# Kernel tuning notes

Measured on AMD Instinct MI355X. Metric: run time of the kernel, lower is better.

## Reference

```python
import jax, jax.numpy as jnp
import numpy as np

B, S, E, H, D, W = 2, 4096, 768, 12, 64, 256  # batch, seq, hidden, heads, head_dim, one-sided window


def setup_inputs() -> dict:
    key = jax.random.key(0)
    ks = jax.random.split(key, 4)
    s = 0.02
    return {
        "hidden_states": jax.random.normal(ks[0], (B, S, E), jnp.float32),
        "Wq": jax.random.normal(ks[1], (E, E), jnp.float32) * s,
        "bq": jnp.zeros((E,), jnp.float32),
        "Wk": jax.random.normal(ks[2], (E, E), jnp.float32) * s,
        "bk": jnp.zeros((E,), jnp.float32),
        "Wv": jax.random.normal(ks[3], (E, E), jnp.float32) * s,
        "bv": jnp.zeros((E,), jnp.float32),
    }


def _band_attention(q, k, v):
    # q,k,v: [B,H,S,D]. Sliding-window attention: query i attends keys j with |j-i| <= W,
    # clipped to [0, S) -- same math as sliding_chunks_matmul_qk + mask_invalid_locations
    # + softmax + sliding_chunks_matmul_pv (dropout p=0, eval mode).
    C = S // W  # number of query chunks of size W

    def ext(x):
        # gather, for each chunk c, the keys of chunks c-1, c, c+1 (zero padded at edges)
        xp = jnp.pad(x, ((0, 0), (0, 0), (W, W), (0, 0)))
        xc = xp.reshape(B, H, C + 2, W, D)
        return jnp.concatenate([xc[:, :, 0:C], xc[:, :, 1:C + 1], xc[:, :, 2:C + 2]], axis=3)  # [B,H,C,3W,D]

    qc = q.reshape(B, H, C, W, D)
    ke = ext(k)
    ve = ext(v)
    scores = jnp.einsum('bhcpd,bhctd->bhcpt', qc, ke)  # [B,H,C,W,3W]

    p = jnp.arange(W)[:, None]            # query offset within chunk
    t = jnp.arange(3 * W)[None, :]        # key offset within extended window
    rel = t - W - p                       # j - i  (relative position)
    j = jnp.arange(C)[:, None, None] * W + (t - W)[None]  # global key index [C,W,3W]
    mask = (jnp.abs(rel)[None] <= W) & (j >= 0) & (j < S)  # band + sequence-boundary mask

    scores = jnp.where(mask[None, None], scores, -1e30)
    probs = jax.nn.softmax(scores, axis=-1)
    out = jnp.einsum('bhcpt,bhctd->bhcpd', probs, ve)
    return out.reshape(B, H, S, D)


def reference(hidden_states, Wq, bq, Wk, bk, Wv, bv):
    scale = 1.0 / float(np.sqrt(D))
    q = (hidden_states @ Wq + bq) * scale  # q scaled by 1/sqrt(head_dim) as in original
    k = hidden_states @ Wk + bk
    v = hidden_states @ Wv + bv
    split = lambda x: x.reshape(B, S, H, D).transpose(0, 2, 1, 3)  # [B,H,S,D]
    out = _band_attention(split(q), split(k), split(v))
    return out.transpose(0, 2, 1, 3).reshape(B, S, E)  # [B,S,E] context_layer
```

## Files before the change

### kernel.cpp

```cpp
#include <hip/hip_runtime.h>

#define BB 2
#define SS 4096
#define EE 768
#define HH 12
#define DD 64
#define WW 256

typedef __attribute__((ext_vector_type(8))) short short8;
typedef __attribute__((ext_vector_type(4))) short short4v;
typedef __attribute__((ext_vector_type(4))) float floatx4;

#define MFMA16(a, b, c) __builtin_amdgcn_mfma_f32_16x16x32_bf16(a, b, c, 0, 0, 0)

__device__ __forceinline__ float bf2f(short x) {
    union { unsigned u; float f; } v;
    v.u = ((unsigned)(unsigned short)x) << 16;
    return v.f;
}

__device__ __forceinline__ short f2bf(float x) {
    union { float f; unsigned u; } v;
    v.f = x;
    unsigned r = v.u + 0x7fffu + ((v.u >> 16) & 1u);
    return (short)(r >> 16);
}

__device__ __forceinline__ float exp2_fast(float x) {
    float r;
    asm("v_exp_f32 %0, %1" : "=v"(r) : "v"(x));
    return r;
}

__device__ __forceinline__ int imin(int a, int b) { return a < b ? a : b; }
__device__ __forceinline__ int imax(int a, int b) { return a > b ? a : b; }

__device__ __forceinline__ void gload_lds16(const short* g, short* l) {
    __builtin_amdgcn_global_load_lds(
        (const __attribute__((address_space(1))) unsigned*)g,
        (__attribute__((address_space(3))) unsigned*)l, 16, 0, 0);
}

__global__ __launch_bounds__(256) void prep(
    const float* __restrict__ hidden, const float* __restrict__ W0,
    const float* __restrict__ W1, const float* __restrict__ W2,
    short* __restrict__ Xb, short* __restrict__ Wt) {
    __shared__ short t[32][33];
    int bid = blockIdx.x;
    int tid = threadIdx.x;
    if (bid < 6144) {
        size_t i4 = (size_t)bid * 256 + tid;
        floatx4 f = *(const floatx4*)(hidden + i4 * 4);
        short4v s;
#pragma unroll
        for (int k = 0; k < 4; k++) s[k] = f2bf(f[k]);
        *(short4v*)(Xb + i4 * 4) = s;
    } else {
        int tmp = bid - 6144;
        int z = tmp / 576, r = tmp % 576;
        int bx = r % 24, by = r / 24;
        const float* in = (z == 0) ? W0 : (z == 1) ? W1 : W2;
        short* op = Wt + (size_t)z * EE * EE;
        int y0 = by * 32;
        int ty = tid >> 3, tx4 = tid & 7;
        floatx4 f = *(const floatx4*)&in[(size_t)(y0 + ty) * EE + bx * 32 + tx4 * 4];
#pragma unroll
        for (int k = 0; k < 4; k++) t[ty][tx4 * 4 + k] = f2bf(f[k]);
        __syncthreads();
        int A = tid >> 3, B0 = (tid & 7) * 4;
        short4v v;
#pragma unroll
        for (int k = 0; k < 4; k++) v[k] = t[B0 + k][A];
        *(short4v*)&op[(size_t)(bx * 32 + A) * EE + y0 + B0] = v;
    }
}

__global__ __launch_bounds__(512) void qkv_gemm(
    const short* __restrict__ Xb, const short* __restrict__ Wt,
    const float* __restrict__ Bq, const float* __restrict__ Bk, const float* __restrict__ Bv,
    short* __restrict__ Qo, short* __restrict__ Ko, short* __restrict__ Vto) {
    int z = blockIdx.z;
    const short* Wz = Wt + (size_t)z * EE * EE;
    const float* bias = (z == 0) ? Bq : (z == 1) ? Bk : Bv;

    __shared__ __align__(16) short As[3][256 * 32];
    __shared__ __align__(16) short Bs[3][128 * 32];
    int tid = threadIdx.x;
    int m0 = blockIdx.x * 256, n0 = blockIdx.y * 128;
    int wave = tid >> 6, lane = tid & 63, lquad = lane >> 4, lrow = lane & 15;
    int wm = (wave >> 1) * 64, wn = (wave & 1) * 64;

    floatx4 acc[4][4] = {};

    int c0 = tid, c1 = 512 + tid;
    int u0 = (c0 & 7) ^ ((c0 >> 3) & 7);
    int r0s = (c0 >> 3) * 2 + (u0 >> 2), q0s = (u0 & 3) * 8;

    const short* xa0 = &Xb[(size_t)(m0 + r0s) * EE + q0s];
    const short* xa1 = xa0 + (size_t)128 * EE;
    const short* wb0 = &Wz[(size_t)(n0 + r0s) * EE + q0s];

    auto issueTile = [&](int t) {
        int k0 = t * 32;
        int bs = t % 3;
        gload_lds16(xa0 + k0, &As[bs][c0 * 8]);
        gload_lds16(xa1 + k0, &As[bs][c1 * 8]);
        gload_lds16(wb0 + k0, &Bs[bs][c0 * 8]);
    };

    int offA[4], offB[4];
#pragma unroll
    for (int mt = 0; mt < 4; mt++) {
        int ra = wm + mt * 16 + lrow;
        int sa = (lquad | ((ra & 1) << 2)) ^ ((ra >> 1) & 7);
        offA[mt] = (ra >> 1) * 64 + sa * 8;
        int rb = wn + mt * 16 + lrow;
        int sb = (lquad | ((rb & 1) << 2)) ^ ((rb >> 1) & 7);
        offB[mt] = (rb >> 1) * 64 + sb * 8;
    }

    issueTile(0);
    issueTile(1);

#pragma unroll
    for (int t = 0; t < 24; ++t) {
        if (t < 23) asm volatile("s_waitcnt vmcnt(3)" ::: "memory");
        else        asm volatile("s_waitcnt vmcnt(0)" ::: "memory");
        __builtin_amdgcn_sched_barrier(0);
        __builtin_amdgcn_s_barrier();
        asm volatile("" ::: "memory");

        if (t + 2 < 24) issueTile(t + 2);

        int bs = t % 3;
        short8 af[4], bfv[4];
#pragma unroll
        for (int mt = 0; mt < 4; mt++)
            af[mt] = *(short8*)&As[bs][offA[mt]];
#pragma unroll
        for (int nt = 0; nt < 4; nt++)
            bfv[nt] = *(short8*)&Bs[bs][offB[nt]];
#pragma unroll
        for (int mt = 0; mt < 4; mt++)
#pragma unroll
            for (int nt = 0; nt < 4; nt++)
                acc[mt][nt] = MFMA16(af[mt], bfv[nt], acc[mt][nt]);
    }

    if (z == 2) {
        for (int nt = 0; nt < 4; nt++) {
            int gn = n0 + wn + nt * 16 + lrow;
            float bv = bias[gn];
            int h = gn >> 6, d = gn & 63;
            for (int mt = 0; mt < 4; mt++) {
                int gm0 = m0 + wm + mt * 16 + lquad * 4;
                int b = gm0 >> 12, s = gm0 & (SS - 1);
                short4v pk;
                for (int r = 0; r < 4; r++) pk[r] = f2bf(acc[mt][nt][r] + bv);
                *(short4v*)&Vto[(((size_t)(b * HH + h)) * DD + d) * SS + s] = pk;
            }
        }
    } else {
        short* out = (z == 0) ? Qo : Ko;
        float scale = (z == 0) ? 0.125f * 1.44269504088896f : 1.0f;
        for (int nt = 0; nt < 4; nt++) {
            int gn = n0 + wn + nt * 16 + lrow;
            float bv = bias[gn];
            int h = gn >> 6, d = gn & 63;
            for (int mt = 0; mt < 4; mt++) {
                int gmb = m0 + wm + mt * 16 + lquad * 4;
                for (int r = 0; r < 4; r++) {
                    int gm = gmb + r;
                    int b = gm >> 12, s = gm & (SS - 1);
                    float v = (acc[mt][nt][r] + bv) * scale;
                    out[(((size_t)(b * HH + h)) * SS + s) * DD + d] = f2bf(v);
                }
            }
        }
    }
}

__global__ __launch_bounds__(256) void band_attn(
    const short* __restrict__ Q, const short* __restrict__ K,
    const short* __restrict__ Vt, float* __restrict__ out) {
    int hb = blockIdx.x;
    int h = hb % HH, b = hb / HH;
    int chunk = blockIdx.y;
    int tid = threadIdx.x;
    int wave = tid >> 6, lane = tid & 63, lquad = lane >> 4, lrow = lane & 15;
    int qbase = chunk * 128 + wave * 32;

    const short* Qh = Q + ((size_t)(b * HH + h)) * SS * DD;
    const short* Kh = K + ((size_t)(b * HH + h)) * SS * DD;
    const short* Vh = Vt + ((size_t)(b * HH + h)) * DD * SS;

    __shared__ __align__(16) short Ks[2][64 * 72];
    __shared__ __align__(16) short Vs[2][64 * 72];
    __shared__ __align__(16) short Ps[4][16 * 72];
    short* Pw = &Ps[wave][0];

    short8 qf[2][2];
#pragma unroll
    for (int m = 0; m < 2; m++)
#pragma unroll
        for (int hh = 0; hh < 2; hh++)
            qf[m][hh] = *(const short8*)&Qh[(size_t)(qbase + m * 16 + lrow) * DD + hh * 32 + lquad * 8];

    floatx4 o[2][4] = {};
    float ls[2] = {0.0f, 0.0f};

    int kwin = chunk * 128 - WW;
    int srow = tid >> 3;
    int scol = (tid & 7) * 8;
    int tlo = wave >> 1;

    short8 kreg[2], vreg[2];
    auto loadTile = [&](int t) {
        int ks0 = kwin + t * 64;
#pragma unroll
        for (int i = 0; i < 2; i++) {
            int r = srow + i * 32;
            int gk = imin(imax(ks0 + r, 0), SS - 1);
            kreg[i] = *(const short8*)&Kh[(size_t)gk * DD + scol];
            int gv = imin(imax(ks0 + scol, 0), SS - 8);
            vreg[i] = *(const short8*)&Vh[(size_t)r * SS + gv];
        }
    };
    auto storeTile = [&](int buf) {
#pragma unroll
        for (int i = 0; i < 2; i++) {
            int r = srow + i * 32;
            *(short8*)&Ks[buf][r * 72 + scol] = kreg[i];
            *(short8*)&Vs[buf][r * 72 + scol] = vreg[i];
        }
    };

    loadTile(0);
    storeTile(0);
    __syncthreads();

    for (int t = 0; t < 10; t++) {
        int buf = t & 1;
        if (t < 9) loadTile(t + 1);

        if ((unsigned)(t - tlo) < 9u) {
            int ks0 = kwin + t * 64;
            short8 kf[4][2], vf[4][2];
#pragma unroll
            for (int kt = 0; kt < 4; kt++)
#pragma unroll
                for (int hh = 0; hh < 2; hh++)
                    kf[kt][hh] = *(short8*)&Ks[buf][(kt * 16 + lrow) * 72 + hh * 32 + lquad * 8];
#pragma unroll
            for (int nt = 0; nt < 4; nt++)
#pragma unroll
                for (int hh = 0; hh < 2; hh++)
                    vf[nt][hh] = *(short8*)&Vs[buf][(nt * 16 + lrow) * 72 + hh * 32 + lquad * 8];

            int d0 = ks0 - qbase;
            bool interior = (d0 >= -225) && (d0 <= 193) && (ks0 >= 0) && (ks0 <= SS - 64);

            __builtin_amdgcn_s_setprio(1);
#pragma unroll
            for (int m = 0; m < 2; m++) {
                int q = qbase + m * 16 + lrow;
                floatx4 s[4];
#pragma unroll
                for (int kt = 0; kt < 4; kt++) {
                    floatx4 zz = {};
                    s[kt] = MFMA16(kf[kt][0], qf[m][0], zz);
                    s[kt] = MFMA16(kf[kt][1], qf[m][1], s[kt]);
                }
                float lacc = 0.0f;
                if (interior) {
#pragma unroll
                    for (int kt = 0; kt < 4; kt++) {
                        short4v pk;
#pragma unroll
                        for (int r = 0; r < 4; r++) {
                            float p = exp2_fast(s[kt][r]);
                            pk[r] = f2bf(p);
                            lacc += bf2f(pk[r]);
                        }
                        *(short4v*)&Pw[lrow * 72 + kt * 16 + lquad * 4] = pk;
                    }
                } else {
#pragma unroll
                    for (int kt = 0; kt < 4; kt++) {
                        short4v pk;
#pragma unroll
                        for (int r = 0; r < 4; r++) {
                            int key = ks0 + kt * 16 + lquad * 4 + r;
                            bool valid = ((unsigned)(key - q + WW) <= 2u * WW) && ((unsigned)key < SS);
                            float p = valid ? exp2_fast(s[kt][r]) : 0.0f;
                            pk[r] = f2bf(p);
                            lacc += bf2f(pk[r]);
                        }
                        *(short4v*)&Pw[lrow * 72 + kt * 16 + lquad * 4] = pk;
                    }
                }
                ls[m] += lacc;
                asm volatile("" ::: "memory");
                short8 ap0 = *(short8*)&Pw[lrow * 72 + lquad * 8];
                short8 ap1 = *(short8*)&Pw[lrow * 72 + 32 + lquad * 8];
#pragma unroll
                for (int nt = 0; nt < 4; nt++) {
                    o[m][nt] = MFMA16(ap0, vf[nt][0], o[m][nt]);
                    o[m][nt] = MFMA16(ap1, vf[nt][1], o[m][nt]);
                }
            }
            __builtin_amdgcn_s_setprio(0);
        }

        if (t < 9) storeTile(buf ^ 1);
        __syncthreads();
    }

#pragma unroll
    for (int m = 0; m < 2; m++) {
        ls[m] += __shfl_xor(ls[m], 16, 64);
        ls[m] += __shfl_xor(ls[m], 32, 64);
        ls[m] = 1.0f / ls[m];
    }

#pragma unroll
    for (int m = 0; m < 2; m++) {
#pragma unroll
        for (int r = 0; r < 4; r++) {
            float linv = __shfl(ls[m], lquad * 4 + r, 64);
            int s = qbase + m * 16 + lquad * 4 + r;
#pragma unroll
            for (int nt = 0; nt < 4; nt++)
                out[((size_t)b * SS + s) * EE + h * DD + nt * 16 + lrow] = o[m][nt][r] * linv;
        }
    }
}

extern "C" void kernel_launch(void* const* d_in, const int* in_sizes, int n_in,
                              void* d_out, int out_size, void* d_ws, size_t ws_size,
                              hipStream_t stream) {
    const float* hidden = (const float*)d_in[0];
    const float* Wq = (const float*)d_in[1];
    const float* bq = (const float*)d_in[2];
    const float* Wk = (const float*)d_in[3];
    const float* bk = (const float*)d_in[4];
    const float* Wv = (const float*)d_in[5];
    const float* bv = (const float*)d_in[6];
    float* out = (float*)d_out;

    short* ws = (short*)d_ws;
    const size_t WSZ = (size_t)EE * EE;
    const size_t QSZ = (size_t)BB * HH * SS * DD;
    short* Wt = ws;
    short* Qb = Wt + 3 * WSZ;
    short* Kb = Qb + QSZ;
    short* Vtb = Kb + QSZ;
    short* Xb = (short*)d_out;

    prep<<<dim3(6144 + 3 * 576, 1, 1), 256, 0, stream>>>(hidden, Wq, Wk, Wv, Xb, Wt);

    qkv_gemm<<<dim3(32, 6, 3), 512, 0, stream>>>(Xb, Wt, bq, bk, bv, Qb, Kb, Vtb);

    band_attn<<<dim3(HH * BB, SS / 128, 1), 256, 0, stream>>>(Qb, Kb, Vtb, out);
}
```

Measured before the change: 173.3 us.

## Use 64-wide K tiles with double buffering in QKV GEMM

The QKV projection GEMM now loads K-tiles of 64 instead of 32 and keeps two LDS buffers instead of three. The swizzle layout is simplified to row-major with an XOR on the 16-byte chunk index. The loop drops to 12 iterations, each waiting for all outstanding loads before computing. This halves the barrier count per tile and doubles the MFMA work between syncs, at the cost of a shallower prefetch depth (one tile ahead, full vmcnt(0) wait) and more LDS per block.

```diff
diff --git a/kernel.cpp b/kernel.cpp
--- a/kernel.cpp
+++ b/kernel.cpp
@@ -83,8 +83,8 @@
     const short* Wz = Wt + (size_t)z * EE * EE;
     const float* bias = (z == 0) ? Bq : (z == 1) ? Bk : Bv;
 
-    __shared__ __align__(16) short As[3][256 * 32];
-    __shared__ __align__(16) short Bs[3][128 * 32];
+    __shared__ __align__(16) short As[2][256 * 64];
+    __shared__ __align__(16) short Bs[2][128 * 64];
     int tid = threadIdx.x;
     int m0 = blockIdx.x * 256, n0 = blockIdx.y * 128;
     int wave = tid >> 6, lane = tid & 63, lquad = lane >> 4, lrow = lane & 15;
@@ -92,59 +92,64 @@
 
     floatx4 acc[4][4] = {};
 
-    int c0 = tid, c1 = 512 + tid;
-    int u0 = (c0 & 7) ^ ((c0 >> 3) & 7);
-    int r0s = (c0 >> 3) * 2 + (u0 >> 2), q0s = (u0 & 3) * 8;
-
-    const short* xa0 = &Xb[(size_t)(m0 + r0s) * EE + q0s];
-    const short* xa1 = xa0 + (size_t)128 * EE;
-    const short* wb0 = &Wz[(size_t)(n0 + r0s) * EE + q0s];
+    int r0 = tid >> 3, q0 = (tid & 7) ^ (r0 & 7);
+    const short* xa0 = &Xb[(size_t)(m0 + r0) * EE + q0 * 8];
+    const short* wb0 = &Wz[(size_t)(n0 + r0) * EE + q0 * 8];
+    int c0 = tid;
 
     auto issueTile = [&](int t) {
-        int k0 = t * 32;
-        int bs = t % 3;
-        gload_lds16(xa0 + k0, &As[bs][c0 * 8]);
-        gload_lds16(xa1 + k0, &As[bs][c1 * 8]);
-        gload_lds16(wb0 + k0, &Bs[bs][c0 * 8]);
+        int k0 = t * 64;
+        int bs = t & 1;
+        gload_lds16(xa0 + k0,            &As[bs][c0 * 8]);
+        gload_lds16(xa0 + 64 * EE + k0,  &As[bs][(c0 + 512) * 8]);
+        gload_lds16(xa0 + 128 * EE + k0, &As[bs][(c0 + 1024) * 8]);
+        gload_lds16(xa0 + 192 * EE + k0, &As[bs][(c0 + 1536) * 8]);
+        gload_lds16(wb0 + k0,            &Bs[bs][c0 * 8]);
+        gload_lds16(wb0 + 64 * EE + k0,  &Bs[bs][(c0 + 512) * 8]);
     };
 
-    int offA[4], offB[4];
+    int offA[4][2], offB[4][2];
 #pragma unroll
     for (int mt = 0; mt < 4; mt++) {
         int ra = wm + mt * 16 + lrow;
-        int sa = (lquad | ((ra & 1) << 2)) ^ ((ra >> 1) & 7);
-        offA[mt] = (ra >> 1) * 64 + sa * 8;
         int rb = wn + mt * 16 + lrow;
-        int sb = (lquad | ((rb & 1) << 2)) ^ ((rb >> 1) & 7);
-        offB[mt] = (rb >> 1) * 64 + sb * 8;
+#pragma unroll
+        for (int hh = 0; hh < 2; hh++) {
+            offA[mt][hh] = ra * 64 + ((hh * 4 + lquad) ^ (ra & 7)) * 8;
+            offB[mt][hh] = rb * 64 + ((hh * 4 + lquad) ^ (rb & 7)) * 8;
+        }
     }
 
     issueTile(0);
-    issueTile(1);
-
-#pragma unroll
-    for (int t = 0; t < 24; ++t) {
-        if (t < 23) asm volatile("s_waitcnt vmcnt(3)" ::: "memory");
-        else        asm volatile("s_waitcnt vmcnt(0)" ::: "memory");
+
+#pragma unroll
+    for (int t = 0; t < 12; ++t) {
+        asm volatile("s_waitcnt vmcnt(0)" ::: "memory");
         __builtin_amdgcn_sched_barrier(0);
         __builtin_amdgcn_s_barrier();
         asm volatile("" ::: "memory");
 
-        if (t + 2 < 24) issueTile(t + 2);
-
-        int bs = t % 3;
-        short8 af[4], bfv[4];
+        if (t + 1 < 12) issueTile(t + 1);
+
+        int bs = t & 1;
+        short8 af[4][2], bfv[4][2];
 #pragma unroll
         for (int mt = 0; mt < 4; mt++)
-            af[mt] = *(short8*)&As[bs][offA[mt]];
+#pragma unroll
+            for (int hh = 0; hh < 2; hh++)
+                af[mt][hh] = *(short8*)&As[bs][offA[mt][hh]];
 #pragma unroll
         for (int nt = 0; nt < 4; nt++)
-            bfv[nt] = *(short8*)&Bs[bs][offB[nt]];
+#pragma unroll
+            for (int hh = 0; hh < 2; hh++)
+                bfv[nt][hh] = *(short8*)&Bs[bs][offB[nt][hh]];
 #pragma unroll
         for (int mt = 0; mt < 4; mt++)
 #pragma unroll
-            for (int nt = 0; nt < 4; nt++)
-                acc[mt][nt] = MFMA16(af[mt], bfv[nt], acc[mt][nt]);
+            for (int nt = 0; nt < 4; nt++) {
+                acc[mt][nt] = MFMA16(af[mt][0], bfv[nt][0], acc[mt][nt]);
+                acc[mt][nt] = MFMA16(af[mt][1], bfv[nt][1], acc[mt][nt]);
+            }
     }
 
     if (z == 2) {
```

After: 181.2 us. 4.6% more time.

## Load K/V tiles directly into LDS with XOR-swizzled layout

Applied to the files above, without the earlier changes.

Replaces the register-staged global loads and LDS stores for K and V tiles with direct global-to-LDS loads (gload_lds16). The padded 72-stride layout is replaced by an XOR-swizzled 64-stride layout to avoid bank conflicts. The pipeline now waits on vmcnt and a barrier at the top of each iteration before issuing the next tile. This removes the VGPR staging and explicit LDS store instructions, but the prefetch now completes via a full vmcnt(0) wait each iteration.

```diff
diff --git a/kernel.cpp b/kernel.cpp
--- a/kernel.cpp
+++ b/kernel.cpp
@@ -194,8 +194,8 @@
     const short* Kh = K + ((size_t)(b * HH + h)) * SS * DD;
     const short* Vh = Vt + ((size_t)(b * HH + h)) * DD * SS;
 
-    __shared__ __align__(16) short Ks[2][64 * 72];
-    __shared__ __align__(16) short Vs[2][64 * 72];
+    __shared__ __align__(16) short Ks[2][64 * 64];
+    __shared__ __align__(16) short Vs[2][64 * 64];
     __shared__ __align__(16) short Ps[4][16 * 72];
     short* Pw = &Ps[wave][0];
 
@@ -210,52 +210,51 @@
     float ls[2] = {0.0f, 0.0f};
 
     int kwin = chunk * 128 - WW;
-    int srow = tid >> 3;
-    int scol = (tid & 7) * 8;
     int tlo = wave >> 1;
 
-    short8 kreg[2], vreg[2];
-    auto loadTile = [&](int t) {
+    int cr0 = tid >> 3, cq0 = (tid & 7) ^ (cr0 & 7);
+    int cr1 = (tid + 256) >> 3, cq1 = (tid & 7) ^ (cr1 & 7);
+
+    auto issueTile = [&](int t) {
         int ks0 = kwin + t * 64;
-#pragma unroll
-        for (int i = 0; i < 2; i++) {
-            int r = srow + i * 32;
-            int gk = imin(imax(ks0 + r, 0), SS - 1);
-            kreg[i] = *(const short8*)&Kh[(size_t)gk * DD + scol];
-            int gv = imin(imax(ks0 + scol, 0), SS - 8);
-            vreg[i] = *(const short8*)&Vh[(size_t)r * SS + gv];
-        }
+        int bs = t & 1;
+        int gk0 = imin(imax(ks0 + cr0, 0), SS - 1);
+        gload_lds16(&Kh[(size_t)gk0 * DD + cq0 * 8], &Ks[bs][tid * 8]);
+        int gk1 = imin(imax(ks0 + cr1, 0), SS - 1);
+        gload_lds16(&Kh[(size_t)gk1 * DD + cq1 * 8], &Ks[bs][(tid + 256) * 8]);
+        int gv0 = imin(imax(ks0 + cq0 * 8, 0), SS - 8);
+        gload_lds16(&Vh[(size_t)cr0 * SS + gv0], &Vs[bs][tid * 8]);
+        int gv1 = imin(imax(ks0 + cq1 * 8, 0), SS - 8);
+        gload_lds16(&Vh[(size_t)cr1 * SS + gv1], &Vs[bs][(tid + 256) * 8]);
     };
-    auto storeTile = [&](int buf) {
-#pragma unroll
-        for (int i = 0; i < 2; i++) {
-            int r = srow + i * 32;
-            *(short8*)&Ks[buf][r * 72 + scol] = kreg[i];
-            *(short8*)&Vs[buf][r * 72 + scol] = vreg[i];
-        }
-    };
-
-    loadTile(0);
-    storeTile(0);
-    __syncthreads();
+
+    int qx0 = lquad ^ (lrow & 7);
+    int qx1 = (4 + lquad) ^ (lrow & 7);
+
+    issueTile(0);
 
     for (int t = 0; t < 10; t++) {
-        int buf = t & 1;
-        if (t < 9) loadTile(t + 1);
+        asm volatile("s_waitcnt vmcnt(0)" ::: "memory");
+        __builtin_amdgcn_sched_barrier(0);
+        __builtin_amdgcn_s_barrier();
+        asm volatile("" ::: "memory");
+
+        if (t < 9) issueTile(t + 1);
 
         if ((unsigned)(t - tlo) < 9u) {
+            int buf = t & 1;
             int ks0 = kwin + t * 64;
             short8 kf[4][2], vf[4][2];
 #pragma unroll
-            for (int kt = 0; kt < 4; kt++)
-#pragma unroll
-                for (int hh = 0; hh < 2; hh++)
-                    kf[kt][hh] = *(short8*)&Ks[buf][(kt * 16 + lrow) * 72 + hh * 32 + lquad * 8];
-#pragma unroll
-            for (int nt = 0; nt < 4; nt++)
-#pragma unroll
-                for (int hh = 0; hh < 2; hh++)
-                    vf[nt][hh] = *(short8*)&Vs[buf][(nt * 16 + lrow) * 72 + hh * 32 + lquad * 8];
+            for (int kt = 0; kt < 4; kt++) {
+                kf[kt][0] = *(short8*)&Ks[buf][(kt * 16 + lrow) * 64 + qx0 * 8];
+                kf[kt][1] = *(short8*)&Ks[buf][(kt * 16 + lrow) * 64 + qx1 * 8];
+            }
+#pragma unroll
+            for (int nt = 0; nt < 4; nt++) {
+                vf[nt][0] = *(short8*)&Vs[buf][(nt * 16 + lrow) * 64 + qx0 * 8];
+                vf[nt][1] = *(short8*)&Vs[buf][(nt * 16 + lrow) * 64 + qx1 * 8];
+            }
 
             int d0 = ks0 - qbase;
             bool interior = (d0 >= -225) && (d0 <= 193) && (ks0 >= 0) && (ks0 <= SS - 64);
@@ -311,9 +310,6 @@
             }
             __builtin_amdgcn_s_setprio(0);
         }
-
-        if (t < 9) storeTile(buf ^ 1);
-        __syncthreads();
     }
 
 #pragma unroll
```

New measurement: 175.1 us. Within noise of the previous version (+1.0%).
